# Kernel tuning notes

Measured on AMD Instinct MI355X. Metric: run time of the kernel, lower is better.

## Reference

```python
import jax, jax.numpy as jnp
import numpy as np
from jax import lax

B, T, D, U = 64, 2048, 512, 32


def setup_inputs() -> dict:
    key = jax.random.key(0)
    k1, k2, k3, k4 = jax.random.split(key, 4)
    x = jax.random.normal(k1, (B, T, D), dtype=jnp.float32)
    # sequence lengths in [1, T]
    nwords = jnp.maximum(jax.random.randint(k2, (B,), 0, T, dtype=jnp.int32), 1)
    kernel = jax.random.normal(k3, (D, U), dtype=jnp.float32) * 0.02
    chain_kernel = jax.random.normal(k4, (U, U), dtype=jnp.float32) * 0.02
    bias = jnp.zeros((U,), dtype=jnp.float32)
    return {"x": x, "nwords": nwords, "kernel": kernel,
            "chain_kernel": chain_kernel, "bias": bias}


def _crf_decode(logits, trans, lengths):
    """Viterbi decode. logits [B,T,U], trans [U,U], lengths [B] int.
    Returns (pred_ids [B,T] int32, best_score [B])."""
    Bb, Tt, Uu = logits.shape
    alpha0 = logits[:, 0]                       # [B,U]
    # valid[t-1, b] = (t < lengths[b]) for t = 1..T-1
    valid = (jnp.arange(1, Tt)[:, None] < lengths[None, :])  # [T-1, B]
    logits_rest = jnp.transpose(logits[:, 1:], (1, 0, 2))    # [T-1, B, U]
    tag_iota = jnp.arange(Uu, dtype=jnp.int32)

    def fwd_step(alpha, inp):
        logit_t, v = inp                        # [B,U], [B]
        scores = alpha[:, :, None] + trans[None, :, :]   # [B, U_prev, U_cur]
        bp = jnp.argmax(scores, axis=1).astype(jnp.int32)  # [B,U]
        new_alpha = jnp.max(scores, axis=1) + logit_t        # [B,U]
        new_alpha = jnp.where(v[:, None], new_alpha, alpha)
        bp = jnp.where(v[:, None], bp, tag_iota[None, :])    # identity at pads
        return new_alpha, bp

    final_alpha, bps = lax.scan(fwd_step, alpha0, (logits_rest, valid))
    # bps: [T-1, B, U]
    last_tag = jnp.argmax(final_alpha, axis=-1).astype(jnp.int32)  # [B]
    best_score = jnp.max(final_alpha, axis=-1)                     # [B]

    def back_step(tag, bp_t):
        prev_tag = jnp.take_along_axis(bp_t, tag[:, None], axis=1)[:, 0]
        return prev_tag, tag

    first_tag, tags_rest = lax.scan(back_step, last_tag, bps, reverse=True)
    # tags_rest[t-1] = tag at time t; first_tag = tag at time 0
    pred = jnp.concatenate([first_tag[None, :], tags_rest], axis=0)  # [T,B]
    return jnp.transpose(pred, (1, 0)), best_score


def reference(x, nwords, kernel, chain_kernel, bias):
    # dense projection (activation = linear, keras default)
    logits = jnp.einsum('btd,du->btu', x, kernel) + bias  # [B,T,U]
    pred_ids, best_score = _crf_decode(logits, chain_kernel, nwords)
    return pred_ids, best_score
```

## Files before the change

### kernel.cpp

```cpp
#include <hip/hip_runtime.h>

#define BB 64
#define TT 2048
#define DD 512
#define UU 32

__device__ int g_ts[BB * 7];
__device__ float g_c[BB * 7];
__device__ float g_bound[BB * 8 * 64];

__global__ __launch_bounds__(256, 4) void k1_logits(const float* __restrict__ x,
                                                    const float* __restrict__ w,
                                                    const float* __restrict__ bias,
                                                    float* __restrict__ out) {
  __shared__ float xs[128 * 34];
  __shared__ float wsh[32 * 36];
  const int tid = threadIdx.x;
  const long row0 = (long)blockIdx.x * 128;
  const int tr = tid >> 2;
  const int tc = tid & 3;
  const int ubase = tc * 8;
  const int sr = tid >> 3;
  const int sc = (tid & 7) * 4;

  float2 acc2[2][4];
#pragma unroll
  for (int i = 0; i < 2; ++i)
#pragma unroll
    for (int j = 0; j < 4; ++j) acc2[i][j] = make_float2(0.0f, 0.0f);

  for (int kc = 0; kc < DD; kc += 32) {
#pragma unroll
    for (int p = 0; p < 4; ++p) {
      const int r = p * 32 + sr;
      const float4 v = *(const float4*)(x + (row0 + r) * DD + kc + sc);
      *(float2*)(&xs[r * 34 + sc]) = make_float2(v.x, v.y);
      *(float2*)(&xs[r * 34 + sc + 2]) = make_float2(v.z, v.w);
    }
    {
      const int k = tid >> 3;
      const int uu4 = (tid & 7) * 4;
      const float4 v = *(const float4*)(w + (size_t)(kc + k) * UU + uu4);
      *(float4*)(&wsh[k * 36 + uu4]) = v;
    }
    __syncthreads();
#pragma unroll
    for (int kp = 0; kp < 16; ++kp) {
      const int k = kp * 2;
      const float4 wa0 = *(const float4*)(&wsh[k * 36 + ubase]);
      const float4 wa1 = *(const float4*)(&wsh[k * 36 + ubase + 4]);
      const float4 wb0 = *(const float4*)(&wsh[(k + 1) * 36 + ubase]);
      const float4 wb1 = *(const float4*)(&wsh[(k + 1) * 36 + ubase + 4]);
#pragma unroll
      for (int i = 0; i < 2; ++i) {
        const float2 xv2 = *(const float2*)(&xs[(tr + 64 * i) * 34 + k]);
        acc2[i][0].x = fmaf(xv2.x, wa0.x, acc2[i][0].x);
        acc2[i][0].y = fmaf(xv2.x, wa0.y, acc2[i][0].y);
        acc2[i][1].x = fmaf(xv2.x, wa0.z, acc2[i][1].x);
        acc2[i][1].y = fmaf(xv2.x, wa0.w, acc2[i][1].y);
        acc2[i][2].x = fmaf(xv2.x, wa1.x, acc2[i][2].x);
        acc2[i][2].y = fmaf(xv2.x, wa1.y, acc2[i][2].y);
        acc2[i][3].x = fmaf(xv2.x, wa1.z, acc2[i][3].x);
        acc2[i][3].y = fmaf(xv2.x, wa1.w, acc2[i][3].y);
        acc2[i][0].x = fmaf(xv2.y, wb0.x, acc2[i][0].x);
        acc2[i][0].y = fmaf(xv2.y, wb0.y, acc2[i][0].y);
        acc2[i][1].x = fmaf(xv2.y, wb0.z, acc2[i][1].x);
        acc2[i][1].y = fmaf(xv2.y, wb0.w, acc2[i][1].y);
        acc2[i][2].x = fmaf(xv2.y, wb1.x, acc2[i][2].x);
        acc2[i][2].y = fmaf(xv2.y, wb1.y, acc2[i][2].y);
        acc2[i][3].x = fmaf(xv2.y, wb1.z, acc2[i][3].x);
        acc2[i][3].y = fmaf(xv2.y, wb1.w, acc2[i][3].y);
      }
    }
    __syncthreads();
  }
  float bv[8];
#pragma unroll
  for (int j = 0; j < 8; ++j) bv[j] = bias[ubase + j];
#pragma unroll
  for (int i = 0; i < 2; ++i) {
    const long row = row0 + tr + 64 * i;
    float4 o0, o1;
    o0.x = acc2[i][0].x + bv[0]; o0.y = acc2[i][0].y + bv[1];
    o0.z = acc2[i][1].x + bv[2]; o0.w = acc2[i][1].y + bv[3];
    o1.x = acc2[i][2].x + bv[4]; o1.y = acc2[i][2].y + bv[5];
    o1.z = acc2[i][3].x + bv[6]; o1.w = acc2[i][3].y + bv[7];
    *(float4*)(out + row * UU + ubase) = o0;
    *(float4*)(out + row * UU + ubase + 4) = o1;
  }
}


#define ROTF(S) \
  __int_as_float(__builtin_amdgcn_update_dpp(0, __float_as_int(P), 0x120 + (S), 0xF, 0xF, true))

#define K2_TREE                                                              \
    const float c0 = P + tvS[0];                                             \
    const float c1 = ROTF(1) + tvS[1];                                       \
    const float c2 = ROTF(2) + tvS[2];                                       \
    const float c3 = ROTF(3) + tvS[3];                                       \
    const float c4 = ROTF(4) + tvS[4];                                       \
    const float c5 = ROTF(5) + tvS[5];                                       \
    const float c6 = ROTF(6) + tvS[6];                                       \
    const float c7 = ROTF(7) + tvS[7];                                       \
    const float c8 = ROTF(8) + tvS[8];                                       \
    const float c9 = ROTF(9) + tvS[9];                                       \
    const float c10 = ROTF(10) + tvS[10];                                    \
    const float c11 = ROTF(11) + tvS[11];                                    \
    const float c12 = ROTF(12) + tvS[12];                                    \
    const float c13 = ROTF(13) + tvS[13];                                    \
    const float c14 = ROTF(14) + tvS[14];                                    \
    const float c15 = ROTF(15) + tvS[15];                                    \
    const float d0 = fmaxf(fmaxf(c0, c1), c2);                               \
    const float d1 = fmaxf(fmaxf(c3, c4), c5);                               \
    const float d2 = fmaxf(fmaxf(c6, c7), c8);                               \
    const float d3 = fmaxf(fmaxf(c9, c10), c11);                             \
    const float d4 = fmaxf(fmaxf(c12, c13), c14);                            \
    const float e0 = fmaxf(fmaxf(d0, d1), d2);                               \
    const float e1 = fmaxf(fmaxf(d3, d4), c15);                              \
    const float pm = fmaxf(e0, e1);

#if __has_builtin(__builtin_amdgcn_permlane32_swap) && __has_builtin(__builtin_amdgcn_permlane16_swap)
#define K2_HAVE_PERMLANE 1
typedef unsigned int v2u __attribute__((ext_vector_type(2)));

#define K2_FSTEP(tval, lg) do {                                              \
    K2_TREE                                                                  \
    v2u s32 = __builtin_amdgcn_permlane32_swap(__float_as_uint(pm),          \
                                               __float_as_uint(pm), false, false); \
    const float pd = fmaxf(__uint_as_float(s32.x), __uint_as_float(s32.y)) + (lg); \
    v2u s16 = __builtin_amdgcn_permlane16_swap(__float_as_uint(pd),          \
                                               __float_as_uint(pd), false, false); \
    const float cx = m16sel ? __uint_as_float(s16.x) : __uint_as_float(s16.y); \
    P = bit5v ? cx : pd;                                                     \
    base[(size_t)(tval) * UU + cstoS] = P;                                   \
  } while (0)

__device__ __forceinline__ float k2_mcomb(float P, const float* tvS) {
  K2_TREE
  v2u s32 = __builtin_amdgcn_permlane32_swap(__float_as_uint(pm),
                                             __float_as_uint(pm), false, false);
  return fmaxf(__uint_as_float(s32.x), __uint_as_float(s32.y));
}

#define K2_RUNSEG(A_, E_) do {                                               \
    int tcc = (A_);                                                          \
    _Pragma("unroll")                                                        \
    for (int i = 0; i < 16; ++i) {                                           \
      int r = (A_) + i; if (r > (E_)) r = (E_);                              \
      bufA[i] = base[(size_t)r * UU + tgtS];                                 \
    }                                                                        \
    _Pragma("unroll 1")                                                      \
    for (; tcc + 31 <= (E_); tcc += 32) {                                    \
      _Pragma("unroll")                                                      \
      for (int i = 0; i < 16; ++i) bufB[i] = base[(size_t)(tcc + 16 + i) * UU + tgtS]; \
      _Pragma("unroll")                                                      \
      for (int i = 0; i < 16; ++i) K2_FSTEP(tcc + i, bufA[i]);               \
      _Pragma("unroll")                                                      \
      for (int i = 0; i < 16; ++i) {                                         \
        int r = tcc + 32 + i; if (r > (E_)) r = (E_);                        \
        bufA[i] = base[(size_t)r * UU + tgtS];                               \
      }                                                                      \
      _Pragma("unroll")                                                      \
      for (int i = 0; i < 16; ++i) K2_FSTEP(tcc + 16 + i, bufB[i]);          \
    }                                                                        \
    const int rem = (E_) - tcc + 1;                                          \
    if (rem > 0) {                                                           \
      _Pragma("unroll")                                                      \
      for (int i = 0; i < 16; ++i) {                                         \
        int r = tcc + 16 + i; if (r > (E_)) r = (E_);                        \
        bufB[i] = base[(size_t)r * UU + tgtS];                               \
      }                                                                      \
      _Pragma("unroll")                                                      \
      for (int i = 0; i < 16; ++i) { if (i < rem) K2_FSTEP(tcc + i, bufA[i]); } \
      _Pragma("unroll")                                                      \
      for (int i = 0; i < 16; ++i) { if (16 + i < rem) K2_FSTEP(tcc + 16 + i, bufB[i]); } \
    }                                                                        \
  } while (0)
#endif

__global__ __launch_bounds__(64) void k2a_forward(float* __restrict__ lb,
                                                  const float* __restrict__ trans) {
  const int lane = threadIdx.x;
  const int q = lane & 15;
  const int bit4 = (lane >> 4) & 1;
  const int bit5v = (lane >> 5) & 1;
  const int hiS = bit4 ^ bit5v;
  const int tgtS = bit4 * 16 + q;
  const int cstoS = hiS * 16 + q;
  const int role = blockIdx.x >> 6;
  const int b = blockIdx.x & 63;

  const int probe = __builtin_amdgcn_update_dpp(0, q, 0x121, 0xF, 0xF, false);
  const bool dirp = (probe == ((q + 1) & 15));

  float tvS[16];
#pragma unroll
  for (int s = 0; s < 16; ++s) {
    const int rp = dirp ? ((q + s) & 15) : ((q - s) & 15);
    tvS[s] = trans[(hiS * 16 + rp) * UU + tgtS];
  }

  float* base = lb + (size_t)b * TT * UU;
  float bufA[16], bufB[16];

#ifdef K2_HAVE_PERMLANE
  v2u p32 = __builtin_amdgcn_permlane32_swap((unsigned)lane, (unsigned)lane, false, false);
  v2u p16 = __builtin_amdgcn_permlane16_swap((unsigned)lane, (unsigned)lane, false, false);
  const bool c32ok = ((int)p32.x == (lane ^ 32)) || ((int)p32.y == (lane ^ 32));
  const bool c16ok = ((int)p16.x == (lane ^ 16)) || ((int)p16.y == (lane ^ 16));
  const bool m16sel = ((int)p16.x == (lane ^ 16));
  const bool okSwap = (__ballot(c32ok) == ~0ull) && (__ballot(c16ok) == ~0ull);

  if (okSwap) {
    if (role == 0) {
      float P = base[cstoS];
      K2_RUNSEG(1, 256);
      g_bound[((b << 3) + 0) * 64 + lane] = P;
    } else {
      const int s0 = 256 * role + 1;
      const int E = (role < 7) ? (256 * (role + 1)) : (TT - 1);
      float P = base[(size_t)s0 * UU + cstoS];
      K2_RUNSEG(s0 + 1, E);
      g_bound[((b << 3) + role) * 64 + lane] = P;
    }
    return;
  }
#endif

  if (role != 0) return;
  {
    float tvD[16];
#pragma unroll
    for (int s = 0; s < 16; ++s) {
      const int rp = dirp ? ((q + s) & 15) : ((q - s) & 15);
      tvD[s] = trans[(bit4 * 16 + rp) * UU + cstoS];
    }
    const int idx32 = (lane ^ 32) << 2;
    const int idx48 = (lane ^ 48) << 2;
    float P = base[cstoS];

#define K2_BSTEP(tval, lg, TVHI, XIDX, SCOL) do {                            \
    const float g0 = P + (TVHI)[0];                                          \
    const float g1 = ROTF(1) + (TVHI)[1];                                    \
    const float g2 = ROTF(2) + (TVHI)[2];                                    \
    const float g3 = ROTF(3) + (TVHI)[3];                                    \
    const float g4 = ROTF(4) + (TVHI)[4];                                    \
    const float g5 = ROTF(5) + (TVHI)[5];                                    \
    const float g6 = ROTF(6) + (TVHI)[6];                                    \
    const float g7 = ROTF(7) + (TVHI)[7];                                    \
    const float g8 = ROTF(8) + (TVHI)[8];                                    \
    const float g9 = ROTF(9) + (TVHI)[9];                                    \
    const float g10 = ROTF(10) + (TVHI)[10];                                 \
    const float g11 = ROTF(11) + (TVHI)[11];                                 \
    const float g12 = ROTF(12) + (TVHI)[12];                                 \
    const float g13 = ROTF(13) + (TVHI)[13];                                 \
    const float g14 = ROTF(14) + (TVHI)[14];                                 \
    const float g15 = ROTF(15) + (TVHI)[15];                                 \
    const float h0 = fmaxf(fmaxf(g0, g1), g2);                               \
    const float h1 = fmaxf(fmaxf(g3, g4), g5);                               \
    const float h2 = fmaxf(fmaxf(g6, g7), g8);                               \
    const float h3 = fmaxf(fmaxf(g9, g10), g11);                             \
    const float h4 = fmaxf(fmaxf(g12, g13), g14);                            \
    const float k0 = fmaxf(fmaxf(h0, h1), h2);                               \
    const float k1 = fmaxf(fmaxf(h3, h4), g15);                              \
    const float pm2 = fmaxf(k0, k1);                                         \
    const int po = __builtin_amdgcn_ds_bpermute((XIDX), __float_as_int(pm2));\
    P = fmaxf(pm2, __int_as_float(po)) + (lg);                               \
    base[(size_t)(tval) * UU + (SCOL)] = P;                                  \
  } while (0)

#pragma unroll
    for (int i = 0; i < 16; ++i)
      bufA[i] = base[(size_t)(1 + i) * UU + ((i & 1) ? cstoS : tgtS)];
#pragma unroll 1
    for (int tc = 1; tc <= 1985; tc += 32) {
#pragma unroll
      for (int i = 0; i < 16; ++i)
        bufB[i] = base[(size_t)(tc + 16 + i) * UU + ((i & 1) ? cstoS : tgtS)];
#pragma unroll
      for (int i = 0; i < 16; ++i) {
        if ((i & 1) == 0) K2_BSTEP(tc + i, bufA[i], tvS, idx32, tgtS);
        else              K2_BSTEP(tc + i, bufA[i], tvD, idx48, cstoS);
      }
#pragma unroll
      for (int i = 0; i < 16; ++i)
        bufA[i] = base[(size_t)(tc + 32 + i) * UU + ((i & 1) ? cstoS : tgtS)];
#pragma unroll
      for (int i = 0; i < 16; ++i) {
        if ((i & 1) == 0) K2_BSTEP(tc + 16 + i, bufB[i], tvS, idx32, tgtS);
        else              K2_BSTEP(tc + 16 + i, bufB[i], tvD, idx48, cstoS);
      }
    }
#pragma unroll
    for (int i = 0; i < 16; ++i) {
      int r = 2033 + i; if (r > TT - 1) r = TT - 1;
      bufB[i] = base[(size_t)r * UU + ((i & 1) ? cstoS : tgtS)];
    }
#pragma unroll
    for (int i = 0; i < 16; ++i) {
      if ((i & 1) == 0) K2_BSTEP(2017 + i, bufA[i], tvS, idx32, tgtS);
      else              K2_BSTEP(2017 + i, bufA[i], tvD, idx48, cstoS);
    }
#pragma unroll
    for (int i = 0; i < 15; ++i) {
      if ((i & 1) == 0) K2_BSTEP(2033 + i, bufB[i], tvS, idx32, tgtS);
      else              K2_BSTEP(2033 + i, bufB[i], tvD, idx48, cstoS);
    }
  }
}

__global__ __launch_bounds__(64) void k2b_fixup(float* __restrict__ lb,
                                                const float* __restrict__ trans) {
  const int lane = threadIdx.x;
  const int b = blockIdx.x & 63;
  const int j = (blockIdx.x >> 6) + 1;
  const int q = lane & 15;
  const int bit4 = (lane >> 4) & 1;
  const int bit5v = (lane >> 5) & 1;
  const int hiS = bit4 ^ bit5v;
  const int tgtS = bit4 * 16 + q;
  const int cstoS = hiS * 16 + q;
  const int jr = 256 * j + 1;
  const int segEnd = (j < 7) ? (256 * (j + 1)) : (TT - 1);

  const int probe = __builtin_amdgcn_update_dpp(0, q, 0x121, 0xF, 0xF, false);
  const bool dirp = (probe == ((q + 1) & 15));

  float tvS[16];
#pragma unroll
  for (int s = 0; s < 16; ++s) {
    const int rp = dirp ? ((q + s) & 15) : ((q - s) & 15);
    tvS[s] = trans[(hiS * 16 + rp) * UU + tgtS];
  }

#ifdef K2_HAVE_PERMLANE
  v2u p32 = __builtin_amdgcn_permlane32_swap((unsigned)lane, (unsigned)lane, false, false);
  v2u p16 = __builtin_amdgcn_permlane16_swap((unsigned)lane, (unsigned)lane, false, false);
  const bool c32ok = ((int)p32.x == (lane ^ 32)) || ((int)p32.y == (lane ^ 32));
  const bool c16ok = ((int)p16.x == (lane ^ 16)) || ((int)p16.y == (lane ^ 16));
  const bool m16sel = ((int)p16.x == (lane ^ 16));
  const bool okSwap = (__ballot(c32ok) == ~0ull) && (__ballot(c16ok) == ~0ull);
  if (!okSwap) {
    if (lane == 0) { g_ts[b * 7 + j - 1] = segEnd; g_c[b * 7 + j - 1] = 0.0f; }
    return;
  }

  float* base = lb + (size_t)b * TT * UU;
  const float TAU = 0.05f;

  float trueP = g_bound[((b << 3) + (j - 1)) * 64 + lane];
  const float specInit = base[(size_t)jr * UU + cstoS];
  const float lgj = base[(size_t)jr * UU + tgtS];
  { float P = trueP; K2_FSTEP(jr, lgj); trueP = P; }
  float specP = specInit;

  float ring[4];
#pragma unroll
  for (int i = 0; i < 4; ++i) {
    int r = jr + 1 + i; if (r > segEnd) r = segEnd;
    ring[i] = base[(size_t)r * UU + cstoS];
  }
  int ts_rec = segEnd; float c_rec = 0.0f;
#pragma unroll 1
  for (int t = jr + 1; t <= segEnd; ++t) {
    const float specRow = ring[(t - (jr + 1)) & 3];
    const int pf = t + 4;
    if (pf <= segEnd) ring[(t - (jr + 1)) & 3] = base[(size_t)pf * UU + cstoS];
    const float Mt = k2_mcomb(trueP, tvS);
    const float Ms = k2_mcomb(specP, tvS);
    const float d = Mt - Ms;
    v2u s16d = __builtin_amdgcn_permlane16_swap(__float_as_uint(d),
                                                __float_as_uint(d), false, false);
    const float dx = m16sel ? __uint_as_float(s16d.x) : __uint_as_float(s16d.y);
    const float dsel = bit5v ? dx : d;
    const float nt = specRow + dsel;
    base[(size_t)t * UU + cstoS] = nt;
    const float dref = __uint_as_float(
        (unsigned)__builtin_amdgcn_readfirstlane(__float_as_int(d)));
    const bool uni = (__ballot(fabsf(d - dref) <= TAU) == ~0ull);
    trueP = nt;
    specP = specRow;
    if (uni) { ts_rec = t; c_rec = dref; break; }
  }
  if (lane == 0) { g_ts[b * 7 + j - 1] = ts_rec; g_c[b * 7 + j - 1] = c_rec; }
#else
  if (lane == 0) { g_ts[b * 7 + j - 1] = segEnd; g_c[b * 7 + j - 1] = 0.0f; }
#endif
}

__global__ __launch_bounds__(256) void k2c_apply(float* __restrict__ lb) {
  const int b = blockIdx.x;
  float C[8];
  C[0] = 0.0f;
#pragma unroll
  for (int j = 1; j <= 7; ++j) C[j] = C[j - 1] + g_c[b * 7 + j - 1];
#pragma unroll 1
  for (int j = 1; j <= 7; ++j) {
    const int jr = 256 * j + 1;
    const int segEnd = (j < 7) ? (256 * (j + 1)) : (TT - 1);
    const int ts = g_ts[b * 7 + j - 1];
    const float cA = C[j - 1];
    const float cB = C[j];
    if (cA != 0.0f) {
      float4* p = (float4*)(lb + ((size_t)b * TT + jr) * UU);
      const int n4 = (ts - jr + 1) * (UU / 4);
      for (int i = threadIdx.x; i < n4; i += 256) {
        float4 v = p[i];
        v.x += cA; v.y += cA; v.z += cA; v.w += cA;
        p[i] = v;
      }
    }
    if (cB != 0.0f && ts < segEnd) {
      float4* p = (float4*)(lb + ((size_t)b * TT + ts + 1) * UU);
      const int n4 = (segEnd - ts) * (UU / 4);
      for (int i = threadIdx.x; i < n4; i += 256) {
        float4 v = p[i];
        v.x += cB; v.y += cB; v.z += cB; v.w += cB;
        p[i] = v;
      }
    }
  }
}

__global__ __launch_bounds__(256) void k3_bp(const float* __restrict__ lb,
                                             const float* __restrict__ trans,
                                             const int* __restrict__ nwords,
                                             unsigned char* __restrict__ bp) {
  __shared__ float as[129 * 32];
  __shared__ float ts[32 * 32];
  const int b = blockIdx.x >> 4;
  const int c = blockIdx.x & 15;
  const int t0 = 128 * c;
  const int tid = threadIdx.x;
  const float* base = lb + (size_t)b * TT * UU;
  const int nw = nwords[b];

  for (int idx = tid; idx < 129 * 32; idx += 256) {
    const int gidx = (t0 - 1) * 32 + idx;
    as[idx] = (gidx >= 0 && gidx < TT * UU) ? base[gidx] : 0.0f;
  }
  for (int idx = tid; idx < 1024; idx += 256) ts[idx] = trans[idx];
  __syncthreads();

  const int u = tid & 31;
  const int tg = tid >> 5;
  unsigned char* bpu = bp + ((size_t)b * 32 + u) * TT;

#pragma unroll 1
  for (int qq = 0; qq < 4; ++qq) {
    const int tl0 = tg * 16 + qq * 4;
    unsigned int pack = 0;
#pragma unroll
    for (int e = 0; e < 4; ++e) {
      const int tl = tl0 + e;
      const int t = t0 + tl;
      int idx;
      if (t >= 1 && t < nw) {
        float m = as[tl * 32 + 0] + ts[0 * 32 + u];
        idx = 0;
#pragma unroll
        for (int v = 1; v < 32; ++v) {
          const float cv = as[tl * 32 + v] + ts[v * 32 + u];
          if (cv > m) { m = cv; idx = v; }
        }
      } else {
        idx = u;
      }
      pack |= ((unsigned int)idx) << (8 * e);
    }
    *(unsigned int*)(bpu + t0 + tl0) = pack;
  }
}

__global__ __launch_bounds__(64) void k4_backtrace(const float* __restrict__ lb,
                                                   const unsigned char* __restrict__ bp,
                                                   const int* __restrict__ nwords,
                                                   int* __restrict__ pred,
                                                   float* __restrict__ score) {
  const int b = blockIdx.x;
  const int lane = threadIdx.x;
  const int u = lane & 31;
  const int h = lane >> 5;
  const int nw = nwords[b];

  const float a = lb[((size_t)b * TT + (nw - 1)) * UU + u];
  float m = a;
#pragma unroll
  for (int s = 32; s; s >>= 1) m = fmaxf(m, __shfl_xor(m, s));
  if (lane == 0) score[b] = m;
  const unsigned long long mask = __ballot(lane < 32 && a == m);
  int tag = __ffsll((unsigned long long)mask) - 1;
  tag = __builtin_amdgcn_readfirstlane(tag);

  int* predb = pred + b * TT;
  for (int p = nw - 1 + lane; p < TT; p += 64) predb[p] = tag;
  if (nw < 2) return;

  const unsigned char* bpb = bp + (size_t)b * 32 * TT;
  const int pcmax = (nw - 2) >> 6;
  const int thi_top = nw - 1;

  int wprev0 = 0;
  {
    const int toff = (pcmax + 1) * 64;
    if (toff < TT) wprev0 = *(const int*)(bpb + (size_t)u * TT + toff);
  }

  for (int pc = pcmax; pc >= 0; --pc) {
    int wreg[8];
#pragma unroll
    for (int j = 0; j < 8; ++j)
      wreg[j] = *(const int*)(bpb + (size_t)u * TT + pc * 64 + 4 * (h * 8 + j));
    int predv = 0;

    if (pc == pcmax) {
      const int thi = thi_top;
      if (pc * 64 + 64 <= thi) {
        const int val = __builtin_amdgcn_readlane(wprev0, tag);
        tag = __builtin_amdgcn_readfirstlane(val & 0xFF);
        if (lane == 63) predv = tag;
      }
#pragma unroll
      for (int lt = 63; lt >= 1; --lt) {
        if (pc * 64 + lt <= thi) {
          const int d = lt >> 2, byte = lt & 3;
          const int hs = d >> 3, j = d & 7;
          const int val = __builtin_amdgcn_readlane(wreg[j], hs * 32 + tag);
          tag = __builtin_amdgcn_readfirstlane((val >> (8 * byte)) & 0xFF);
          if (lane == lt - 1) predv = tag;
        }
      }
      const int lim = thi - pc * 64;
      if (lane < lim) predb[pc * 64 + lane] = predv;
    } else {
      {
        const int val = __builtin_amdgcn_readlane(wprev0, tag);
        tag = __builtin_amdgcn_readfirstlane(val & 0xFF);
        if (lane == 63) predv = tag;
      }
#pragma unroll
      for (int lt = 63; lt >= 1; --lt) {
        const int d = lt >> 2, byte = lt & 3;
        const int hs = d >> 3, j = d & 7;
        const int val = __builtin_amdgcn_readlane(wreg[j], hs * 32 + tag);
        tag = __builtin_amdgcn_readfirstlane((val >> (8 * byte)) & 0xFF);
        if (lane == lt - 1) predv = tag;
      }
      predb[pc * 64 + lane] = predv;
    }
    wprev0 = wreg[0];
  }
}

extern "C" void kernel_launch(void* const* d_in, const int* in_sizes, int n_in,
                              void* d_out, int out_size, void* d_ws, size_t ws_size,
                              hipStream_t stream) {
  const float* x = (const float*)d_in[0];
  const int* nwords = (const int*)d_in[1];
  const float* kern = (const float*)d_in[2];
  const float* chain = (const float*)d_in[3];
  const float* bias = (const float*)d_in[4];

  float* logits = (float*)d_ws;
  unsigned char* bp = (unsigned char*)d_ws + (size_t)BB * TT * UU * 4;

  int* pred = (int*)d_out;
  float* score = (float*)d_out + (size_t)BB * TT;

  k1_logits<<<dim3(1024), dim3(256), 0, stream>>>(x, kern, bias, logits);
  k2a_forward<<<dim3(512), dim3(64), 0, stream>>>(logits, chain);
  k2b_fixup<<<dim3(448), dim3(64), 0, stream>>>(logits, chain);
  k2c_apply<<<dim3(BB), dim3(256), 0, stream>>>(logits);
  k3_bp<<<dim3(BB * 16), dim3(256), 0, stream>>>(logits, chain, nwords, bp);
  k4_backtrace<<<dim3(BB), dim3(64), 0, stream>>>(logits, bp, nwords, pred, score);
}
```

Before: 192.2 us.

## Fuse segment offset correction into consumers and enlarge logits GEMM row tile

```diff
diff --git a/kernel.cpp b/kernel.cpp
--- a/kernel.cpp
+++ b/kernel.cpp
@@ -9,29 +9,29 @@
 __device__ float g_c[BB * 7];
 __device__ float g_bound[BB * 8 * 64];
 
-__global__ __launch_bounds__(256, 4) void k1_logits(const float* __restrict__ x,
-                                                    const float* __restrict__ w,
-                                                    const float* __restrict__ bias,
-                                                    float* __restrict__ out) {
-  __shared__ float xs[128 * 34];
+__global__ __launch_bounds__(256) void k1_logits(const float* __restrict__ x,
+                                                 const float* __restrict__ w,
+                                                 const float* __restrict__ bias,
+                                                 float* __restrict__ out) {
+  __shared__ float xs[256 * 34];
   __shared__ float wsh[32 * 36];
   const int tid = threadIdx.x;
-  const long row0 = (long)blockIdx.x * 128;
+  const long row0 = (long)blockIdx.x * 256;
   const int tr = tid >> 2;
   const int tc = tid & 3;
   const int ubase = tc * 8;
   const int sr = tid >> 3;
   const int sc = (tid & 7) * 4;
 
-  float2 acc2[2][4];
-#pragma unroll
-  for (int i = 0; i < 2; ++i)
-#pragma unroll
-    for (int j = 0; j < 4; ++j) acc2[i][j] = make_float2(0.0f, 0.0f);
+  float acc[4][8];
+#pragma unroll
+  for (int i = 0; i < 4; ++i)
+#pragma unroll
+    for (int j = 0; j < 8; ++j) acc[i][j] = 0.0f;
 
   for (int kc = 0; kc < DD; kc += 32) {
 #pragma unroll
-    for (int p = 0; p < 4; ++p) {
+    for (int p = 0; p < 8; ++p) {
       const int r = p * 32 + sr;
       const float4 v = *(const float4*)(x + (row0 + r) * DD + kc + sc);
       *(float2*)(&xs[r * 34 + sc]) = make_float2(v.x, v.y);
@@ -51,25 +51,15 @@
       const float4 wa1 = *(const float4*)(&wsh[k * 36 + ubase + 4]);
       const float4 wb0 = *(const float4*)(&wsh[(k + 1) * 36 + ubase]);
       const float4 wb1 = *(const float4*)(&wsh[(k + 1) * 36 + ubase + 4]);
-#pragma unroll
-      for (int i = 0; i < 2; ++i) {
+      const float wva[8] = {wa0.x, wa0.y, wa0.z, wa0.w, wa1.x, wa1.y, wa1.z, wa1.w};
+      const float wvb[8] = {wb0.x, wb0.y, wb0.z, wb0.w, wb1.x, wb1.y, wb1.z, wb1.w};
+#pragma unroll
+      for (int i = 0; i < 4; ++i) {
         const float2 xv2 = *(const float2*)(&xs[(tr + 64 * i) * 34 + k]);
-        acc2[i][0].x = fmaf(xv2.x, wa0.x, acc2[i][0].x);
-        acc2[i][0].y = fmaf(xv2.x, wa0.y, acc2[i][0].y);
-        acc2[i][1].x = fmaf(xv2.x, wa0.z, acc2[i][1].x);
-        acc2[i][1].y = fmaf(xv2.x, wa0.w, acc2[i][1].y);
-        acc2[i][2].x = fmaf(xv2.x, wa1.x, acc2[i][2].x);
-        acc2[i][2].y = fmaf(xv2.x, wa1.y, acc2[i][2].y);
-        acc2[i][3].x = fmaf(xv2.x, wa1.z, acc2[i][3].x);
-        acc2[i][3].y = fmaf(xv2.x, wa1.w, acc2[i][3].y);
-        acc2[i][0].x = fmaf(xv2.y, wb0.x, acc2[i][0].x);
-        acc2[i][0].y = fmaf(xv2.y, wb0.y, acc2[i][0].y);
-        acc2[i][1].x = fmaf(xv2.y, wb0.z, acc2[i][1].x);
-        acc2[i][1].y = fmaf(xv2.y, wb0.w, acc2[i][1].y);
-        acc2[i][2].x = fmaf(xv2.y, wb1.x, acc2[i][2].x);
-        acc2[i][2].y = fmaf(xv2.y, wb1.y, acc2[i][2].y);
-        acc2[i][3].x = fmaf(xv2.y, wb1.z, acc2[i][3].x);
-        acc2[i][3].y = fmaf(xv2.y, wb1.w, acc2[i][3].y);
+#pragma unroll
+        for (int j = 0; j < 8; ++j) acc[i][j] = fmaf(xv2.x, wva[j], acc[i][j]);
+#pragma unroll
+        for (int j = 0; j < 8; ++j) acc[i][j] = fmaf(xv2.y, wvb[j], acc[i][j]);
       }
     }
     __syncthreads();
@@ -78,13 +68,13 @@
 #pragma unroll
   for (int j = 0; j < 8; ++j) bv[j] = bias[ubase + j];
 #pragma unroll
-  for (int i = 0; i < 2; ++i) {
+  for (int i = 0; i < 4; ++i) {
     const long row = row0 + tr + 64 * i;
     float4 o0, o1;
-    o0.x = acc2[i][0].x + bv[0]; o0.y = acc2[i][0].y + bv[1];
-    o0.z = acc2[i][1].x + bv[2]; o0.w = acc2[i][1].y + bv[3];
-    o1.x = acc2[i][2].x + bv[4]; o1.y = acc2[i][2].y + bv[5];
-    o1.z = acc2[i][3].x + bv[6]; o1.w = acc2[i][3].y + bv[7];
+    o0.x = acc[i][0] + bv[0]; o0.y = acc[i][1] + bv[1];
+    o0.z = acc[i][2] + bv[2]; o0.w = acc[i][3] + bv[3];
+    o1.x = acc[i][4] + bv[4]; o1.y = acc[i][5] + bv[5];
+    o1.z = acc[i][6] + bv[6]; o1.w = acc[i][7] + bv[7];
     *(float4*)(out + row * UU + ubase) = o0;
     *(float4*)(out + row * UU + ubase + 4) = o1;
   }
@@ -389,39 +379,6 @@
 #endif
 }
 
-__global__ __launch_bounds__(256) void k2c_apply(float* __restrict__ lb) {
-  const int b = blockIdx.x;
-  float C[8];
-  C[0] = 0.0f;
-#pragma unroll
-  for (int j = 1; j <= 7; ++j) C[j] = C[j - 1] + g_c[b * 7 + j - 1];
-#pragma unroll 1
-  for (int j = 1; j <= 7; ++j) {
-    const int jr = 256 * j + 1;
-    const int segEnd = (j < 7) ? (256 * (j + 1)) : (TT - 1);
-    const int ts = g_ts[b * 7 + j - 1];
-    const float cA = C[j - 1];
-    const float cB = C[j];
-    if (cA != 0.0f) {
-      float4* p = (float4*)(lb + ((size_t)b * TT + jr) * UU);
-      const int n4 = (ts - jr + 1) * (UU / 4);
-      for (int i = threadIdx.x; i < n4; i += 256) {
-        float4 v = p[i];
-        v.x += cA; v.y += cA; v.z += cA; v.w += cA;
-        p[i] = v;
-      }
-    }
-    if (cB != 0.0f && ts < segEnd) {
-      float4* p = (float4*)(lb + ((size_t)b * TT + ts + 1) * UU);
-      const int n4 = (segEnd - ts) * (UU / 4);
-      for (int i = threadIdx.x; i < n4; i += 256) {
-        float4 v = p[i];
-        v.x += cB; v.y += cB; v.z += cB; v.w += cB;
-        p[i] = v;
-      }
-    }
-  }
-}
 
 __global__ __launch_bounds__(256) void k3_bp(const float* __restrict__ lb,
                                              const float* __restrict__ trans,
@@ -436,9 +393,26 @@
   const float* base = lb + (size_t)b * TT * UU;
   const int nw = nwords[b];
 
+  float C[8];
+  int TS[8];
+  C[0] = 0.0f; TS[0] = 0;
+#pragma unroll
+  for (int j = 1; j <= 7; ++j) {
+    C[j] = C[j - 1] + g_c[b * 7 + j - 1];
+    TS[j] = g_ts[b * 7 + j - 1];
+  }
+
   for (int idx = tid; idx < 129 * 32; idx += 256) {
     const int gidx = (t0 - 1) * 32 + idx;
-    as[idx] = (gidx >= 0 && gidx < TT * UU) ? base[gidx] : 0.0f;
+    float v = 0.0f;
+    if (gidx >= 0 && gidx < TT * UU) {
+      const int row = (t0 - 1) + (idx >> 5);
+      const int jj = (row - 1) >> 8;
+      float off = 0.0f;
+      if (jj >= 1) off = (row <= TS[jj]) ? C[jj - 1] : C[jj];
+      v = base[gidx] + off;
+    }
+    as[idx] = v;
   }
   for (int idx = tid; idx < 1024; idx += 256) ts[idx] = trans[idx];
   __syncthreads();
@@ -484,7 +458,23 @@
   const int h = lane >> 5;
   const int nw = nwords[b];
 
-  const float a = lb[((size_t)b * TT + (nw - 1)) * UU + u];
+  float off = 0.0f;
+  {
+    const int row = nw - 1;
+    const int jj = (row - 1) >> 8;
+    if (jj >= 1) {
+      float Cacc = 0.0f;
+      float Cprev = 0.0f;
+#pragma unroll
+      for (int j = 1; j <= 7; ++j) {
+        Cprev = Cacc;
+        Cacc += g_c[b * 7 + j - 1];
+        if (j == jj) off = (row <= g_ts[b * 7 + j - 1]) ? Cprev : Cacc;
+      }
+    }
+  }
+
+  const float a = lb[((size_t)b * TT + (nw - 1)) * UU + u] + off;
   float m = a;
 #pragma unroll
   for (int s = 32; s; s >>= 1) m = fmaxf(m, __shfl_xor(m, s));
@@ -568,10 +558,9 @@
   int* pred = (int*)d_out;
   float* score = (float*)d_out + (size_t)BB * TT;
 
-  k1_logits<<<dim3(1024), dim3(256), 0, stream>>>(x, kern, bias, logits);
+  k1_logits<<<dim3(512), dim3(256), 0, stream>>>(x, kern, bias, logits);
   k2a_forward<<<dim3(512), dim3(64), 0, stream>>>(logits, chain);
   k2b_fixup<<<dim3(448), dim3(64), 0, stream>>>(logits, chain);
-  k2c_apply<<<dim3(BB), dim3(256), 0, stream>>>(logits);
   k3_bp<<<dim3(BB * 16), dim3(256), 0, stream>>>(logits, chain, nwords, bp);
   k4_backtrace<<<dim3(BB), dim3(64), 0, stream>>>(logits, bp, nwords, pred, score);
 }
```

Result: faster. 178.8 us (-7.0%).
